# Performance work log

Hardware: AMD Instinct MI355X
Metric: run time of the kernel (lower is better)

The kernel has to match this reference:

```python
import jax, jax.numpy as jnp
import numpy as np

L = 8          # num_layers
D = 128        # state_dim
B = 8192       # batch
P = L * (L - 1) // 2  # 28 layer pairs
EPS = 1e-12
ALPHA = 0.1    # quantum info mixing coefficient
NOISE = 0.01


def setup_inputs() -> dict:
    key = jax.random.key(0)
    ks = jax.random.split(key, 6)
    return {
        "layer_states": jax.random.normal(ks[0], (L, B, D), jnp.float32),
        "ent_strengths": jax.random.normal(ks[1], (L, L), jnp.float32) * 0.7,
        "W1": jax.random.normal(ks[2], (P, 2 * D, 2 * D), jnp.float32) * 0.05,
        "b1": jax.random.normal(ks[3], (P, 2 * D), jnp.float32) * 0.05,
        "W2": jax.random.normal(ks[4], (P, 2 * D, 2 * D), jnp.float32) * 0.05,
        "b2": jax.random.normal(ks[5], (P, 2 * D), jnp.float32) * 0.05,
    }


def _entropy_rank1(v, d):
    # von Neumann entropy of rho = vn vn^T (rank-1 symmetric): eigvals = (|vn|^2, 0,...,0)
    # matches torch eigvals path with clamp(min=1e-12) analytically.
    n = jnp.sqrt(jnp.sum(v * v, axis=-1, keepdims=True))
    vn = v / jnp.maximum(n, EPS)                      # F.normalize(p=2, eps=1e-12)
    lam1 = jnp.clip(jnp.sum(vn * vn, axis=-1), EPS, None)
    zero_term = -(d - 1) * EPS * np.log(EPS)          # (d-1) clamped zero eigenvalues
    return -(lam1 * jnp.log(lam1)) + zero_term


def reference(layer_states, ent_strengths, W1, b1, W2, b2):
    ii, jj = np.triu_indices(L, k=1)                  # pair order matches the python double loop
    s_i = layer_states[ii]                            # [P,B,D]
    s_j = layer_states[jj]                            # [P,B,D]
    comb = jnp.concatenate([s_i, s_j], axis=-1)       # [P,B,2D]

    # batched per-pair Bell MLP: Linear -> Tanh -> Linear
    h = jnp.tanh(jnp.einsum('pbd,pde->pbe', comb, W1) + b1[:, None, :])
    bell = jnp.einsum('pbd,pde->pbe', h, W2) + b2[:, None, :]

    strength = jax.nn.sigmoid(ent_strengths[ii, jj])  # [P]
    noise = NOISE * jax.random.normal(jax.random.key(42), bell.shape, bell.dtype)
    ent = strength[:, None, None] * bell + noise      # [P,B,2D]

    # quantum mutual information I = S1 + S2 - S12 (rank-1 density matrices)
    measures = _entropy_rank1(s_i, D) + _entropy_rank1(s_j, D) - _entropy_rank1(ent, 2 * D)  # [P,B]

    # sequential propagation: u_k <- u_k + alpha*(e_k - u_k), in global pair order
    updated = [layer_states[k] for k in range(L)]
    for p in range(P):
        i, j = int(ii[p]), int(jj[p])
        updated[i] = updated[i] + ALPHA * (ent[p, :, :D] - updated[i])
        updated[j] = updated[j] + ALPHA * (ent[p, :, D:] - updated[j])
    updated = jnp.stack(updated, axis=0)              # [L,B,D]

    return updated, measures
```

## Files before the change

kernel.cpp:

```cpp
#include <hip/hip_runtime.h>
#include <math.h>

#define L_ 8
#define D_ 128
#define B_ 8192
#define P_ 28
#define ALPHA_ 0.1f

typedef __attribute__((ext_vector_type(8))) short bf16x8;
typedef __attribute__((ext_vector_type(4))) float f32x4;
union BF8 { int4 i; bf16x8 h; short s[8]; };

__device__ __forceinline__ short f2bf(float f) {
    unsigned u = __float_as_uint(f);
    unsigned r = (u + 0x7fffu + ((u >> 16) & 1u)) >> 16;
    return (short)(r & 0xffffu);
}
__device__ __forceinline__ unsigned rne2(float a, float b) {
    unsigned ua = __float_as_uint(a); ua += 0x7fffu + ((ua >> 16) & 1u);
    unsigned ub = __float_as_uint(b); ub += 0x7fffu + ((ub >> 16) & 1u);
    return __builtin_amdgcn_perm(ub, ua, 0x07060302);
}
__device__ __forceinline__ unsigned cvt_pk_bf16(float lo, float hi) {
    unsigned r;
    asm("v_cvt_pk_bf16_f32 %0, %1, %2" : "=v"(r) : "v"(lo), "v"(hi));
    return r;
}
__device__ __forceinline__ float fast_tanh(float x) {
    float e = exp2f(x * 2.885390081777927f);
    return 1.f - 2.f * __builtin_amdgcn_rcpf(e + 1.f);
}

__global__ void transpose_w(const float* __restrict__ W1, const float* __restrict__ W2,
                            short* __restrict__ T1, short* __restrict__ T2) {
    const float* W = blockIdx.y ? W2 : W1;
    short* T = blockIdx.y ? T2 : T1;
    const int p = blockIdx.x >> 3, kb = blockIdx.x & 7;
    __shared__ float tile[32][260];
    const int tid = threadIdx.x;
    for (int s = tid; s < 8192; s += 256) {
        int kk = s >> 8, n = s & 255;
        tile[kk][n] = W[((size_t)p * 256 + kb * 32 + kk) * 256 + n];
    }
    __syncthreads();
    const int n = tid;
    const int ch = n >> 7, ct = (n >> 4) & 7, mm = n & 15;
    const size_t sb = (((size_t)p * 2 + ch) * 64 + kb * 8) * 512;
    short tmp[32];
#pragma unroll
    for (int kk = 0; kk < 32; ++kk) tmp[kk] = f2bf(tile[kk][n]);
#pragma unroll
    for (int c4 = 0; c4 < 4; ++c4) {
        BF8 u;
#pragma unroll
        for (int e = 0; e < 8; ++e) u.s[e] = tmp[c4 * 8 + e];
        const int byt = ct * 1024 + mm * 64 + c4 * 16;
        *(int4*)&T[sb + (byt >> 1)] = u.i;
    }
}

__global__ void prep_s16(const float* __restrict__ S, short* __restrict__ S16) {
    __shared__ __align__(16) short ls[8192];
    const int t = threadIdx.x;
    const size_t base = (size_t)blockIdx.x * 8192;
#pragma unroll
    for (int rr = 0; rr < 8; ++rr) {
        const int idx = rr * 1024 + t * 4;
        const float4 v = *(const float4*)&S[base + idx];
        const int row = idx >> 7, col = idx & 127;
        const int rgl = row >> 4, mr = row & 15, kq = col >> 3, c4 = (col >> 2) & 1;
        const unsigned w0 = rne2(v.x, v.y), w1 = rne2(v.z, v.w);
        const int byt = (rgl * 4096 + kq * 256 + mr * 16 + c4 * 8) ^ ((kq & 7) << 4);
        *(uint2*)((char*)ls + byt) = (uint2){w0, w1};
    }
    __syncthreads();
#pragma unroll
    for (int r = 0; r < 4; ++r) {
        const int un = r * 256 + t;
        const int kq = (un >> 4) & 15;
        const int byt = (un * 16) ^ ((kq & 7) << 4);
        *(int4*)&S16[base + (size_t)un * 8] = *(const int4*)((const char*)ls + byt);
    }
}

__launch_bounds__(512, 4)
__global__ void fused(const float* __restrict__ S, const float* __restrict__ ES,
                      const float* __restrict__ b1, const float* __restrict__ b2,
                      const short* __restrict__ S16, const short* __restrict__ T1,
                      const short* __restrict__ T2, float* __restrict__ OUT) {
    __shared__ __align__(16) short Hs[32768];
    const int k = blockIdx.x, rb = blockIdx.y;
    const int tid = threadIdx.x, lane = tid & 63, w = tid >> 6;
    const int wr = w >> 2, wc = w & 3;
    const int m = lane & 15, q = lane >> 4;
    char* const hsb = (char*)Hs;
    const int afo = wc * 1024 + m * 32 + q * 8;

    const size_t srow = (size_t)k * B_ + rb * 128;

    f32x4 acc2[2][4];
    float st_prev = 1.f;

    for (int it = 0; it < 7; ++it) {
        const int mp = it + (it >= k ? 1 : 0);
        const int li = k < mp ? k : mp;
        const int lj = k < mp ? mp : k;
        const int p  = li * 7 - ((li * (li - 1)) >> 1) + (lj - li - 1);
        const int side = (k == li) ? 0 : 1;
        const float es = ES[li * L_ + lj];
        const float st = 1.f / (1.f + expf(-es));
        const float ratio = 0.9f * st_prev / st;

#pragma unroll
        for (int at = 0; at < 2; ++at) {
            const f32x4 bv = *(const f32x4*)&b2[p * 256 + side * 128 + wc * 32 + at * 16 + q * 4];
#pragma unroll
            for (int nt = 0; nt < 4; ++nt)
#pragma unroll
                for (int r = 0; r < 4; ++r)
                    acc2[at][nt][r] = (it == 0) ? bv[r] : acc2[at][nt][r] * ratio + bv[r];
        }
        st_prev = st;

        const short* biL = S16 + ((size_t)li * 512 + rb * 8 + wr * 4) * 2048 + (q * 16 + m) * 8;
        const size_t dJ = (size_t)(lj - li) * 512 * 2048;

        for (int hh = 0; hh < 2; ++hh) {
            const short* wA = T1 + ((size_t)(p * 2 + hh) << 15) + afo;
            f32x4 acc1[2][4];
#pragma unroll
            for (int at = 0; at < 2; ++at) {
                const f32x4 bv = *(const f32x4*)&b1[p * 256 + hh * 128 + wc * 32 + at * 16 + q * 4];
#pragma unroll
                for (int nt = 0; nt < 4; ++nt) acc1[at][nt] = bv;
            }
#pragma unroll
            for (int kb = 0; kb < 8; ++kb) {
                const short* sp = biL + ((kb < 4) ? 0 : dJ) + (kb & 3) * 512;
                const bf16x8 A0 = *(const bf16x8*)(wA + kb * 4096);
                const bf16x8 A1 = *(const bf16x8*)(wA + kb * 4096 + 512);
#pragma unroll
                for (int nt = 0; nt < 4; ++nt) {
                    const bf16x8 Bf = *(const bf16x8*)(sp + nt * 2048);
                    acc1[0][nt] = __builtin_amdgcn_mfma_f32_16x16x32_bf16(A0, Bf, acc1[0][nt], 0, 0, 0);
                    acc1[1][nt] = __builtin_amdgcn_mfma_f32_16x16x32_bf16(A1, Bf, acc1[1][nt], 0, 0, 0);
                }
            }
#pragma unroll
            for (int at = 0; at < 2; ++at) {
                const int cb = (hh * 16 + wc * 4 + at * 2 + (q >> 1)) * 256 + m * 16 + (q & 1) * 8;
#pragma unroll
                for (int nt = 0; nt < 4; ++nt) {
                    const float v0 = fast_tanh(acc1[at][nt][0]);
                    const float v1 = fast_tanh(acc1[at][nt][1]);
                    const float v2 = fast_tanh(acc1[at][nt][2]);
                    const float v3 = fast_tanh(acc1[at][nt][3]);
                    const unsigned p0 = cvt_pk_bf16(v0, v1);
                    const unsigned p1 = cvt_pk_bf16(v2, v3);
                    *(uint2*)(hsb + (wr * 4 + nt) * 8192 + cb) = (uint2){p0, p1};
                }
            }
        }
        __syncthreads();

        const short* wA2 = T2 + ((size_t)(p * 2 + side) << 15) + afo;
#pragma unroll
        for (int kb = 0; kb < 8; ++kb) {
            const bf16x8 A0 = *(const bf16x8*)(wA2 + kb * 4096);
            const bf16x8 A1 = *(const bf16x8*)(wA2 + kb * 4096 + 512);
            const int hc = (kb * 4 + q) * 256 + m * 16;
#pragma unroll
            for (int nt = 0; nt < 4; ++nt) {
                const bf16x8 Hf = *(const bf16x8*)(hsb + (wr * 4 + nt) * 8192 + hc);
                acc2[0][nt] = __builtin_amdgcn_mfma_f32_16x16x32_bf16(A0, Hf, acc2[0][nt], 0, 0, 0);
                acc2[1][nt] = __builtin_amdgcn_mfma_f32_16x16x32_bf16(A1, Hf, acc2[1][nt], 0, 0, 0);
            }
        }
        __syncthreads();
    }

    const float fin = 0.1f * st_prev;
#pragma unroll
    for (int nt = 0; nt < 4; ++nt)
#pragma unroll
        for (int at = 0; at < 2; ++at) {
            const size_t off = (srow + wr * 64 + nt * 16 + m) * D_ + wc * 32 + at * 16 + q * 4;
            const f32x4 u0 = *(const f32x4*)&S[off];
            f32x4 o;
#pragma unroll
            for (int r = 0; r < 4; ++r)
                o[r] = 0.4782969f * u0[r] + fin * acc2[at][nt][r];
            *(f32x4*)&OUT[off] = o;
        }
}

__global__ void fill_meas(float* __restrict__ M) {
    int t = blockIdx.x * 256 + threadIdx.x;
    if (t < P_ * B_) M[t] = -2.7631021115928547e-11f;
}

extern "C" void kernel_launch(void* const* d_in, const int* in_sizes, int n_in,
                              void* d_out, int out_size, void* d_ws, size_t ws_size,
                              hipStream_t stream) {
    const float* S  = (const float*)d_in[0];
    const float* ES = (const float*)d_in[1];
    const float* W1 = (const float*)d_in[2];
    const float* b1 = (const float*)d_in[3];
    const float* W2 = (const float*)d_in[4];
    const float* b2 = (const float*)d_in[5];

    short* S16 = (short*)d_ws;
    short* T1  = S16 + (size_t)L_ * B_ * D_;
    short* T2  = T1 + (size_t)P_ * 2 * 32768;

    float* OUT  = (float*)d_out;
    float* MEAS = OUT + (size_t)L_ * B_ * D_;

    transpose_w<<<dim3(P_ * 8, 2), 256, 0, stream>>>(W1, W2, T1, T2);
    prep_s16<<<dim3(1024), 256, 0, stream>>>(S, S16);
    fused<<<dim3(8, 64), 512, 0, stream>>>(S, ES, b1, b2, S16, T1, T2, OUT);
    fill_meas<<<dim3(896), 256, 0, stream>>>(MEAS);
}
```

Measured before the change: 280.4 us.

## Halve fused block rows, stage state tiles in LDS via async loads

Blocks now cover 64 rows with 4 waves instead of 128 rows with 8 waves, which doubles the grid to 1024 blocks. The block's own layer-state tile and the partner tile are copied into LDS with global_load_lds, and the next partner tile is prefetched during the second GEMM. The hidden activations are processed in two 128-wide halves, each consumed right away by the second GEMM, which cuts the H buffer to 16 KB. The goals are to avoid re-reading bf16 state from global memory on every k-block and to improve occupancy. The cost is more barriers per iteration and twice as many reads of the weight tiles across blocks.

```diff
diff --git a/kernel.cpp b/kernel.cpp
--- a/kernel.cpp
+++ b/kernel.cpp
@@ -30,6 +30,9 @@
     float e = exp2f(x * 2.885390081777927f);
     return 1.f - 2.f * __builtin_amdgcn_rcpf(e + 1.f);
 }
+
+typedef const unsigned int __attribute__((address_space(1)))* gas_t;
+typedef unsigned int __attribute__((address_space(3)))* las_t;
 
 __global__ void transpose_w(const float* __restrict__ W1, const float* __restrict__ W2,
                             short* __restrict__ T1, short* __restrict__ T2) {
@@ -83,20 +86,38 @@
     }
 }
 
-__launch_bounds__(512, 4)
+__device__ __forceinline__ void stage16k(const short* __restrict__ src, short* dst,
+                                         int w, int lane) {
+#pragma unroll
+    for (int r = 0; r < 4; ++r) {
+        const int u0 = (w * 4 + r) * 64;
+        __builtin_amdgcn_global_load_lds((gas_t)(const void*)(src + (size_t)(u0 + lane) * 8),
+                                         (las_t)(void*)(dst + u0 * 8), 16, 0, 0);
+    }
+}
+
+__launch_bounds__(256, 4)
 __global__ void fused(const float* __restrict__ S, const float* __restrict__ ES,
                       const float* __restrict__ b1, const float* __restrict__ b2,
                       const short* __restrict__ S16, const short* __restrict__ T1,
                       const short* __restrict__ T2, float* __restrict__ OUT) {
-    __shared__ __align__(16) short Hs[32768];
+    __shared__ __align__(16) short Sown[8192];
+    __shared__ __align__(16) short Spar[8192];
+    __shared__ __align__(16) short Hh[8192];
     const int k = blockIdx.x, rb = blockIdx.y;
-    const int tid = threadIdx.x, lane = tid & 63, w = tid >> 6;
-    const int wr = w >> 2, wc = w & 3;
+    const int tid = threadIdx.x, lane = tid & 63, wc = tid >> 6;
     const int m = lane & 15, q = lane >> 4;
-    char* const hsb = (char*)Hs;
+    char* const hsb = (char*)Hh;
     const int afo = wc * 1024 + m * 32 + q * 8;
-
-    const size_t srow = (size_t)k * B_ + rb * 128;
+    const int bfo = (q * 16 + m) * 8;
+
+    const size_t srow = (size_t)k * B_ + rb * 64;
+
+    stage16k(S16 + ((size_t)k * 512 + rb * 4) * 2048, Sown, wc, lane);
+    {
+        const int mp0 = (0 >= k) ? 1 : 0;
+        stage16k(S16 + ((size_t)mp0 * 512 + rb * 4) * 2048, Spar, wc, lane);
+    }
 
     f32x4 acc2[2][4];
     float st_prev = 1.f;
@@ -122,8 +143,7 @@
         }
         st_prev = st;
 
-        const short* biL = S16 + ((size_t)li * 512 + rb * 8 + wr * 4) * 2048 + (q * 16 + m) * 8;
-        const size_t dJ = (size_t)(lj - li) * 512 * 2048;
+        __syncthreads();
 
         for (int hh = 0; hh < 2; ++hh) {
             const short* wA = T1 + ((size_t)(p * 2 + hh) << 15) + afo;
@@ -136,7 +156,8 @@
             }
 #pragma unroll
             for (int kb = 0; kb < 8; ++kb) {
-                const short* sp = biL + ((kb < 4) ? 0 : dJ) + (kb & 3) * 512;
+                const short* lsrc = ((kb < 4) == (side == 0)) ? Sown : Spar;
+                const short* sp = lsrc + (kb & 3) * 512 + bfo;
                 const bf16x8 A0 = *(const bf16x8*)(wA + kb * 4096);
                 const bf16x8 A1 = *(const bf16x8*)(wA + kb * 4096 + 512);
 #pragma unroll
@@ -148,7 +169,7 @@
             }
 #pragma unroll
             for (int at = 0; at < 2; ++at) {
-                const int cb = (hh * 16 + wc * 4 + at * 2 + (q >> 1)) * 256 + m * 16 + (q & 1) * 8;
+                const int cb = (wc * 4 + at * 2 + (q >> 1)) * 256 + m * 16 + (q & 1) * 8;
 #pragma unroll
                 for (int nt = 0; nt < 4; ++nt) {
                     const float v0 = fast_tanh(acc1[at][nt][0]);
@@ -157,26 +178,32 @@
                     const float v3 = fast_tanh(acc1[at][nt][3]);
                     const unsigned p0 = cvt_pk_bf16(v0, v1);
                     const unsigned p1 = cvt_pk_bf16(v2, v3);
-                    *(uint2*)(hsb + (wr * 4 + nt) * 8192 + cb) = (uint2){p0, p1};
+                    *(uint2*)(hsb + nt * 4096 + cb) = (uint2){p0, p1};
                 }
             }
+            __syncthreads();
+
+            if (hh == 1 && it < 6) {
+                const int mp2 = (it + 1) + ((it + 1) >= k ? 1 : 0);
+                stage16k(S16 + ((size_t)mp2 * 512 + rb * 4) * 2048, Spar, wc, lane);
+            }
+
+            const short* wA2 = T2 + ((size_t)(p * 2 + side) << 15) + afo;
+#pragma unroll
+            for (int kc = 0; kc < 4; ++kc) {
+                const int kb = hh * 4 + kc;
+                const bf16x8 A0 = *(const bf16x8*)(wA2 + kb * 4096);
+                const bf16x8 A1 = *(const bf16x8*)(wA2 + kb * 4096 + 512);
+                const int hc = (kc * 4 + q) * 256 + m * 16;
+#pragma unroll
+                for (int nt = 0; nt < 4; ++nt) {
+                    const bf16x8 Hf = *(const bf16x8*)(hsb + nt * 4096 + hc);
+                    acc2[0][nt] = __builtin_amdgcn_mfma_f32_16x16x32_bf16(A0, Hf, acc2[0][nt], 0, 0, 0);
+                    acc2[1][nt] = __builtin_amdgcn_mfma_f32_16x16x32_bf16(A1, Hf, acc2[1][nt], 0, 0, 0);
+                }
+            }
+            if (hh == 0) __syncthreads();
         }
-        __syncthreads();
-
-        const short* wA2 = T2 + ((size_t)(p * 2 + side) << 15) + afo;
-#pragma unroll
-        for (int kb = 0; kb < 8; ++kb) {
-            const bf16x8 A0 = *(const bf16x8*)(wA2 + kb * 4096);
-            const bf16x8 A1 = *(const bf16x8*)(wA2 + kb * 4096 + 512);
-            const int hc = (kb * 4 + q) * 256 + m * 16;
-#pragma unroll
-            for (int nt = 0; nt < 4; ++nt) {
-                const bf16x8 Hf = *(const bf16x8*)(hsb + (wr * 4 + nt) * 8192 + hc);
-                acc2[0][nt] = __builtin_amdgcn_mfma_f32_16x16x32_bf16(A0, Hf, acc2[0][nt], 0, 0, 0);
-                acc2[1][nt] = __builtin_amdgcn_mfma_f32_16x16x32_bf16(A1, Hf, acc2[1][nt], 0, 0, 0);
-            }
-        }
-        __syncthreads();
     }
 
     const float fin = 0.1f * st_prev;
@@ -184,7 +211,7 @@
     for (int nt = 0; nt < 4; ++nt)
 #pragma unroll
         for (int at = 0; at < 2; ++at) {
-            const size_t off = (srow + wr * 64 + nt * 16 + m) * D_ + wc * 32 + at * 16 + q * 4;
+            const size_t off = (srow + nt * 16 + m) * D_ + wc * 32 + at * 16 + q * 4;
             const f32x4 u0 = *(const f32x4*)&S[off];
             f32x4 o;
 #pragma unroll
@@ -218,6 +245,6 @@
 
     transpose_w<<<dim3(P_ * 8, 2), 256, 0, stream>>>(W1, W2, T1, T2);
     prep_s16<<<dim3(1024), 256, 0, stream>>>(S, S16);
-    fused<<<dim3(8, 64), 512, 0, stream>>>(S, ES, b1, b2, S16, T1, T2, OUT);
+    fused<<<dim3(8, 128), 256, 0, stream>>>(S, ES, b1, b2, S16, T1, T2, OUT);
     fill_meas<<<dim3(896), 256, 0, stream>>>(MEAS);
 }
```

Measured after the change: 256.9 us. -8.4%, faster.
